# Kernel optimization log

Hardware: AMD Instinct MI355X
Metric: run time of the kernel (lower is better)

Reference implementation:

```python
import jax, jax.numpy as jnp
import numpy as np

B, T, C, H = 8, 1024, 768, 12
D = C // H  # head_dim = 64

def _rope_tables(seq_len, d, base=10000.0):
    inv_freq = 1.0 / (base ** (jnp.arange(0, d, 2, dtype=jnp.float32) / d))  # [d/2]
    freqs = jnp.outer(jnp.arange(seq_len, dtype=jnp.float32), inv_freq)      # [T, d/2]
    return jnp.cos(freqs), jnp.sin(freqs)

def _apply_rotary(x, cos, sin):
    # x: [B,T,H,D]; cos/sin: [1,T,1,D/2]
    d = x.shape[-1] // 2
    x1, x2 = x[..., :d], x[..., d:]
    return jnp.concatenate([x1 * cos + x2 * sin, -x1 * sin + x2 * cos], axis=-1)

def setup_inputs() -> dict:
    key = jax.random.key(0)
    k1, k2, k3 = jax.random.split(key, 3)
    x = jax.random.normal(k1, (B, T, C), dtype=jnp.float32)
    w_qkv = jax.random.normal(k2, (3 * C, C), dtype=jnp.float32) * (C ** -0.5)
    w_proj = jax.random.normal(k3, (C, C), dtype=jnp.float32) * (C ** -0.5)
    return {"x": x, "w_qkv": w_qkv, "w_proj": w_proj}

def reference(x, w_qkv, w_proj):
    Bb, Tt, Cc = x.shape
    qkv = x @ w_qkv.T                                   # [B,T,3C]
    q, k, v = jnp.split(qkv, 3, axis=2)
    q = q.reshape(Bb, Tt, H, D)
    k = k.reshape(Bb, Tt, H, D)
    v = v.reshape(Bb, Tt, H, D)
    cos, sin = _rope_tables(Tt, D)
    cos = cos[None, :, None, :]
    sin = sin[None, :, None, :]
    q = _apply_rotary(q, cos, sin)
    k = _apply_rotary(k, cos, sin)
    scale = 1.0 / jnp.sqrt(jnp.float32(D))
    scores = jnp.einsum('bthd,bshd->bhts', q, k) * scale  # [B,H,T,T]
    causal = jnp.tril(jnp.ones((Tt, Tt), dtype=bool))
    scores = jnp.where(causal[None, None], scores, jnp.finfo(scores.dtype).min)
    p = jax.nn.softmax(scores, axis=-1)
    y = jnp.einsum('bhts,bshd->bthd', p, v).reshape(Bb, Tt, Cc)
    return y @ w_proj.T
```

## Files before the change

### kernel.cpp

```cpp
#include <hip/hip_runtime.h>
#include <hip/hip_bf16.h>

#define Bb 8
#define Tt 1024
#define Cc 768
#define Hh 12
#define Dd 64
#define M_ROWS (Bb * Tt)
#define QKV_N (3 * Cc)

typedef __attribute__((ext_vector_type(8))) short s16x8;
typedef __attribute__((ext_vector_type(4))) short s16x4;
typedef __attribute__((ext_vector_type(4))) float f32x4;

static __device__ __forceinline__ short f2bf(float f) {
    union { float f; unsigned u; } v; v.f = f;
    unsigned r = (v.u + 0x7fffu + ((v.u >> 16) & 1u)) >> 16;
    return (short)r;
}

__global__ __launch_bounds__(256) void cast_bf16(const float* __restrict__ in,
                                                 short* __restrict__ out, int n8) {
    int i = blockIdx.x * blockDim.x + threadIdx.x;
    if (i >= n8) return;
    const float4 a = ((const float4*)in)[i * 2];
    const float4 b = ((const float4*)in)[i * 2 + 1];
    s16x8 f;
    f[0] = f2bf(a.x); f[1] = f2bf(a.y); f[2] = f2bf(a.z); f[3] = f2bf(a.w);
    f[4] = f2bf(b.x); f[5] = f2bf(b.y); f[6] = f2bf(b.z); f[7] = f2bf(b.w);
    ((s16x8*)out)[i] = f;
}

__global__ __launch_bounds__(256) void rope_tables(float2* __restrict__ cs) {
    int idx = blockIdx.x * blockDim.x + threadIdx.x;
    int t = idx >> 5, i = idx & 31;
    float inv_freq = exp2f(-0.41524101186092037f * (float)i);
    float fr = (float)t * inv_freq;
    float2 v; v.x = cosf(fr); v.y = sinf(fr);
    cs[idx] = v;
}

template <int MODE>
__global__ __launch_bounds__(256) void gemm_nt_mfma(const short* __restrict__ A,
                                                    const short* __restrict__ B,
                                                    void* __restrict__ Cout,
                                                    const float2* __restrict__ cs,
                                                    int M, int N, int K) {
    __shared__ short As[128 * 32];
    __shared__ short Bs[128 * 32];

    const int wave = threadIdx.x >> 6;
    const int lane = threadIdx.x & 63;
    const int l16  = lane & 15;
    const int quad = lane >> 4;
    const int wm = (wave >> 1) * 64;
    const int wn = (wave & 1) * 64;
    const int bm = blockIdx.y * 128;
    const int bn = blockIdx.x * 128;

    f32x4 acc[4][4] = {};

    for (int k0 = 0; k0 < K; k0 += 32) {
        __syncthreads();
#pragma unroll
        for (int i = 0; i < 2; i++) {
            const int idx = (wave * 2 + i) * 64 + lane;
            const int row = idx >> 2;
            const int kc  = (idx & 3) * 8;
            const short* ga = A + (size_t)(bm + row) * K + k0 + kc;
            const short* gb = B + (size_t)(bn + row) * K + k0 + kc;
            __builtin_amdgcn_global_load_lds(
                (const __attribute__((address_space(1))) unsigned*)ga,
                (__attribute__((address_space(3))) unsigned*)&As[(wave * 2 + i) * 512],
                16, 0, 0);
            __builtin_amdgcn_global_load_lds(
                (const __attribute__((address_space(1))) unsigned*)gb,
                (__attribute__((address_space(3))) unsigned*)&Bs[(wave * 2 + i) * 512],
                16, 0, 0);
        }
        __syncthreads();

        s16x8 af[4], bfr[4];
#pragma unroll
        for (int mt = 0; mt < 4; mt++)
            af[mt] = *(const s16x8*)&As[(wm + mt * 16 + l16) * 32 + quad * 8];
#pragma unroll
        for (int nt = 0; nt < 4; nt++)
            bfr[nt] = *(const s16x8*)&Bs[(wn + nt * 16 + l16) * 32 + quad * 8];
#pragma unroll
        for (int mt = 0; mt < 4; mt++)
#pragma unroll
            for (int nt = 0; nt < 4; nt++)
                acc[mt][nt] = __builtin_amdgcn_mfma_f32_16x16x32_bf16(
                    af[mt], bfr[nt], acc[mt][nt], 0, 0, 0);
    }

    if constexpr (MODE == 0) {
#pragma unroll
        for (int mt = 0; mt < 4; mt++)
#pragma unroll
            for (int r = 0; r < 4; r++) {
                const size_t row = bm + wm + mt * 16 + quad * 4 + r;
#pragma unroll
                for (int nt = 0; nt < 4; nt++)
                    ((float*)Cout)[row * N + bn + wn + nt * 16 + l16] = acc[mt][nt][r];
            }
    } else {
        const bool is_v = (bn >= 2 * Cc);
        if (is_v) {
#pragma unroll
            for (int mt = 0; mt < 4; mt++)
#pragma unroll
                for (int r = 0; r < 4; r++) {
                    const size_t row = bm + wm + mt * 16 + quad * 4 + r;
#pragma unroll
                    for (int nt = 0; nt < 4; nt++)
                        ((short*)Cout)[row * N + bn + wn + nt * 16 + l16] = f2bf(acc[mt][nt][r]);
                }
        } else {
            const float scale = (bn < Cc) ? 0.125f : 1.0f;
#pragma unroll
            for (int mt = 0; mt < 4; mt++) {
#pragma unroll
                for (int r = 0; r < 4; r++) {
                    const int row = bm + wm + mt * 16 + quad * 4 + r;
                    const int t = row & (Tt - 1);
                    const float2 c0 = cs[t * 32 + l16];
                    const float2 c1 = cs[t * 32 + 16 + l16];
                    const float x0 = acc[mt][0][r], x1 = acc[mt][1][r];
                    const float x2 = acc[mt][2][r], x3 = acc[mt][3][r];
                    short* cp = (short*)Cout + (size_t)row * N + bn + wn;
                    cp[l16]      = f2bf((x0 * c0.x + x2 * c0.y) * scale);
                    cp[16 + l16] = f2bf((x1 * c1.x + x3 * c1.y) * scale);
                    cp[32 + l16] = f2bf((-x0 * c0.y + x2 * c0.x) * scale);
                    cp[48 + l16] = f2bf((-x1 * c1.y + x3 * c1.x) * scale);
                }
            }
        }
    }
}

#define KSP 72
#define VSP 72
#define PP  76

__global__ __launch_bounds__(256) void flash_attn(const short* __restrict__ qkv,
                                                  short* __restrict__ y) {
    __shared__ short Ks[2][64 * KSP];
    __shared__ short Vs[2][Dd * VSP];
    __shared__ short Ps[4][16 * PP];

    const int wave = threadIdx.x >> 6;
    const int lane = threadIdx.x & 63;
    const int l16  = lane & 15;
    const int quad = lane >> 4;

    const int pair = blockIdx.x / 96;
    const int bh   = blockIdx.x % 96;
    const int h = bh % Hh;
    const int b = bh / Hh;
    const int qa_blk = pair;
    const int qb_blk = 15 - pair;
    const int q0a = qa_blk * 64 + wave * 16;
    const int q0b = qb_blk * 64 + wave * 16;

    s16x8 qfa[2], qfb[2];
    {
        const short* qpa = qkv + (size_t)(b * Tt + q0a + l16) * QKV_N + h * Dd + quad * 8;
        const short* qpb = qkv + (size_t)(b * Tt + q0b + l16) * QKV_N + h * Dd + quad * 8;
        qfa[0] = *(const s16x8*)qpa;  qfa[1] = *(const s16x8*)(qpa + 32);
        qfb[0] = *(const s16x8*)qpb;  qfb[1] = *(const s16x8*)(qpb + 32);
    }

    f32x4 oa[4] = {}, ob[4] = {};
    float la[4] = {0.f, 0.f, 0.f, 0.f}, lb[4] = {0.f, 0.f, 0.f, 0.f};

    short* pw = &Ps[wave][0];

    const int krow = threadIdx.x >> 2;
    const int kd0  = (threadIdx.x & 3) * 16;
    const int key2 = (threadIdx.x & 31) * 2;
    const int dv0  = (threadIdx.x >> 5) * 8;

    s16x8 pk0, pk1, pv0, pv1;
    auto load_tile = [&](int kbase) {
        const short* kp = qkv + (size_t)(b * Tt + kbase + krow) * QKV_N + Cc + h * Dd + kd0;
        pk0 = *(const s16x8*)kp;
        pk1 = *(const s16x8*)(kp + 8);
        const short* vp = qkv + (size_t)(b * Tt + kbase + key2) * QKV_N + 2 * Cc + h * Dd + dv0;
        pv0 = *(const s16x8*)vp;
        pv1 = *(const s16x8*)(vp + QKV_N);
    };
    auto store_tile = [&](int buf) {
        *(s16x8*)&Ks[buf][krow * KSP + kd0]     = pk0;
        *(s16x8*)&Ks[buf][krow * KSP + kd0 + 8] = pk1;
#pragma unroll
        for (int j = 0; j < 8; j++) {
            ushort2 w; w.x = (unsigned short)pv0[j]; w.y = (unsigned short)pv1[j];
            *(ushort2*)&Vs[buf][(dv0 + j) * VSP + key2] = w;
        }
    };

    auto process = [&](int buf, int q0, const s16x8* qf, f32x4* o, float* l_r,
                       int kbase, bool masked) {
        f32x4 sv[4];
#pragma unroll
        for (int g = 0; g < 4; g++) {
            s16x8 kf0 = *(const s16x8*)&Ks[buf][(g * 16 + l16) * KSP + quad * 8];
            s16x8 kf1 = *(const s16x8*)&Ks[buf][(g * 16 + l16) * KSP + 32 + quad * 8];
            f32x4 z = {};
            z = __builtin_amdgcn_mfma_f32_16x16x32_bf16(qf[0], kf0, z, 0, 0, 0);
            z = __builtin_amdgcn_mfma_f32_16x16x32_bf16(qf[1], kf1, z, 0, 0, 0);
            sv[g] = z;
        }
#pragma unroll
        for (int r = 0; r < 4; r++) {
            const int qg = q0 + quad * 4 + r;
            float rs = 0.f;
#pragma unroll
            for (int g = 0; g < 4; g++) {
                float p = __expf(sv[g][r]);
                if (masked) p = (kbase + g * 16 + l16 <= qg) ? p : 0.0f;
                rs += p;
                pw[(quad * 4 + r) * PP + g * 16 + l16] = f2bf(p);
            }
            l_r[r] += rs;
        }
#pragma unroll
        for (int c = 0; c < 2; c++) {
            s16x4 plo = *(const s16x4*)&pw[l16 * PP + c * 32 + quad * 8];
            s16x4 phi = *(const s16x4*)&pw[l16 * PP + c * 32 + quad * 8 + 4];
            s16x8 pa = __builtin_shufflevector(plo, phi, 0, 1, 2, 3, 4, 5, 6, 7);
#pragma unroll
            for (int nc = 0; nc < 4; nc++) {
                s16x8 vb = *(const s16x8*)&Vs[buf][(nc * 16 + l16) * VSP + c * 32 + quad * 8];
                o[nc] = __builtin_amdgcn_mfma_f32_16x16x32_bf16(pa, vb, o[nc], 0, 0, 0);
            }
        }
    };

    load_tile(0);
    store_tile(0);
    for (int kt = 0; kt <= qb_blk; kt++) {
        __syncthreads();
        const int nb = (kt < qb_blk) ? (kt + 1) * 64 : qb_blk * 64;
        load_tile(nb);
        const int buf = kt & 1;
        const int kbase = kt * 64;
        process(buf, q0b, qfb, ob, lb, kbase, kt == qb_blk);
        if (kt <= qa_blk)
            process(buf, q0a, qfa, oa, la, kbase, kt == qa_blk);
        store_tile(buf ^ 1);
    }

#pragma unroll
    for (int r = 0; r < 4; r++) {
        float sa = la[r], sb = lb[r];
#pragma unroll
        for (int off = 1; off < 16; off <<= 1) {
            sa += __shfl_xor(sa, off, 64);
            sb += __shfl_xor(sb, off, 64);
        }
        const float inva = 1.0f / sa;
        const float invb = 1.0f / sb;
        short* ypa = y + (size_t)(b * Tt + q0a + quad * 4 + r) * Cc + h * Dd;
        short* ypb = y + (size_t)(b * Tt + q0b + quad * 4 + r) * Cc + h * Dd;
#pragma unroll
        for (int nc = 0; nc < 4; nc++) {
            ypa[nc * 16 + l16] = f2bf(oa[nc][r] * inva);
            ypb[nc * 16 + l16] = f2bf(ob[nc][r] * invb);
        }
    }
}

extern "C" void kernel_launch(void* const* d_in, const int* in_sizes, int n_in,
                              void* d_out, int out_size, void* d_ws, size_t ws_size,
                              hipStream_t stream) {
    const float* x      = (const float*)d_in[0];
    const float* w_qkv  = (const float*)d_in[1];
    const float* w_proj = (const float*)d_in[2];
    float* out = (float*)d_out;

    float2* cs    = (float2*)d_ws;
    short* xb     = (short*)(cs + Tt * 32);
    short* wqkvb  = xb + (size_t)M_ROWS * Cc;
    short* wprojb = wqkvb + (size_t)QKV_N * Cc;
    short* qkvb   = wprojb + (size_t)Cc * Cc;
    short* yb     = qkvb + (size_t)M_ROWS * QKV_N;

    cast_bf16<<<(M_ROWS * Cc / 8 + 255) / 256, 256, 0, stream>>>(x, xb, M_ROWS * Cc / 8);
    cast_bf16<<<(QKV_N * Cc / 8 + 255) / 256, 256, 0, stream>>>(w_qkv, wqkvb, QKV_N * Cc / 8);
    cast_bf16<<<(Cc * Cc / 8 + 255) / 256, 256, 0, stream>>>(w_proj, wprojb, Cc * Cc / 8);
    rope_tables<<<(Tt * 32) / 256, 256, 0, stream>>>(cs);

    gemm_nt_mfma<1><<<dim3(QKV_N / 128, M_ROWS / 128), 256, 0, stream>>>(
        xb, wqkvb, qkvb, cs, M_ROWS, QKV_N, Cc);

    flash_attn<<<96 * 8, 256, 0, stream>>>(qkvb, yb);

    gemm_nt_mfma<0><<<dim3(Cc / 128, M_ROWS / 128), 256, 0, stream>>>(
        yb, wprojb, out, nullptr, M_ROWS, Cc, Cc);
}
```

Before: 199.8 us.

## Fuse prep kernels, deepen GEMM K-tile with swizzled LDS, and remap blocks per XCD

The three bf16 casts and the RoPE table build are merged into one prep kernel, saving launch overhead. Both GEMMs now stage 64-wide K tiles instead of 32, with an XOR swizzle on the LDS column to avoid bank conflicts. They also use a 1D grid remapped so each XCD owns a contiguous band of M row-blocks, for better L2 locality. The larger tiles double LDS use per block, which may lower occupancy, and the attention kernel is unchanged.

```diff
diff --git a/kernel.cpp b/kernel.cpp
--- a/kernel.cpp
+++ b/kernel.cpp
@@ -19,10 +19,8 @@
     return (short)r;
 }
 
-__global__ __launch_bounds__(256) void cast_bf16(const float* __restrict__ in,
-                                                 short* __restrict__ out, int n8) {
-    int i = blockIdx.x * blockDim.x + threadIdx.x;
-    if (i >= n8) return;
+static __device__ __forceinline__ void cast8(const float* __restrict__ in,
+                                             short* __restrict__ out, int i) {
     const float4 a = ((const float4*)in)[i * 2];
     const float4 b = ((const float4*)in)[i * 2 + 1];
     s16x8 f;
@@ -31,13 +29,33 @@
     ((s16x8*)out)[i] = f;
 }
 
-__global__ __launch_bounds__(256) void rope_tables(float2* __restrict__ cs) {
+#define S1 (M_ROWS * Cc / 8)
+#define S2 (QKV_N * Cc / 8)
+#define S3 (Cc * Cc / 8)
+#define SROPE (Tt * 32)
+#define PREP_THREADS (S1 + S2 + S3 + SROPE)
+
+__global__ __launch_bounds__(256) void prep_kernel(const float* __restrict__ x,
+                                                   const float* __restrict__ wqkv,
+                                                   const float* __restrict__ wproj,
+                                                   short* __restrict__ xb,
+                                                   short* __restrict__ wqkvb,
+                                                   short* __restrict__ wprojb,
+                                                   float2* __restrict__ cs) {
     int idx = blockIdx.x * blockDim.x + threadIdx.x;
-    int t = idx >> 5, i = idx & 31;
-    float inv_freq = exp2f(-0.41524101186092037f * (float)i);
-    float fr = (float)t * inv_freq;
-    float2 v; v.x = cosf(fr); v.y = sinf(fr);
-    cs[idx] = v;
+    if (idx < S1) { cast8(x, xb, idx); return; }
+    idx -= S1;
+    if (idx < S2) { cast8(wqkv, wqkvb, idx); return; }
+    idx -= S2;
+    if (idx < S3) { cast8(wproj, wprojb, idx); return; }
+    idx -= S3;
+    {
+        int t = idx >> 5, i = idx & 31;
+        float inv_freq = exp2f(-0.41524101186092037f * (float)i);
+        float fr = (float)t * inv_freq;
+        float2 v; v.x = cosf(fr); v.y = sinf(fr);
+        cs[idx] = v;
+    }
 }
 
 template <int MODE>
@@ -45,9 +63,9 @@
                                                     const short* __restrict__ B,
                                                     void* __restrict__ Cout,
                                                     const float2* __restrict__ cs,
-                                                    int M, int N, int K) {
-    __shared__ short As[128 * 32];
-    __shared__ short Bs[128 * 32];
+                                                    int M, int N, int K, int nblocks) {
+    __shared__ short As[128 * 64];
+    __shared__ short Bs[128 * 64];
 
     const int wave = threadIdx.x >> 6;
     const int lane = threadIdx.x & 63;
@@ -55,44 +73,53 @@
     const int quad = lane >> 4;
     const int wm = (wave >> 1) * 64;
     const int wn = (wave & 1) * 64;
-    const int bm = blockIdx.y * 128;
-    const int bn = blockIdx.x * 128;
+
+    const int mb8  = (M >> 7) >> 3;
+    const int xcd  = blockIdx.x & 7;
+    const int slot = blockIdx.x >> 3;
+    const int bm = (xcd * mb8 + slot / nblocks) * 128;
+    const int bn = (slot % nblocks) * 128;
 
     f32x4 acc[4][4] = {};
 
-    for (int k0 = 0; k0 < K; k0 += 32) {
+    for (int k0 = 0; k0 < K; k0 += 64) {
         __syncthreads();
 #pragma unroll
-        for (int i = 0; i < 2; i++) {
-            const int idx = (wave * 2 + i) * 64 + lane;
-            const int row = idx >> 2;
-            const int kc  = (idx & 3) * 8;
-            const short* ga = A + (size_t)(bm + row) * K + k0 + kc;
-            const short* gb = B + (size_t)(bn + row) * K + k0 + kc;
+        for (int j = 0; j < 4; j++) {
+            const int idx = (j * 4 + wave) * 64 + lane;
+            const int row = idx >> 3;
+            const int kc  = (((idx & 7) ^ ((idx >> 3) & 7)) * 8);
             __builtin_amdgcn_global_load_lds(
-                (const __attribute__((address_space(1))) unsigned*)ga,
-                (__attribute__((address_space(3))) unsigned*)&As[(wave * 2 + i) * 512],
+                (const __attribute__((address_space(1))) unsigned*)
+                    (A + (size_t)(bm + row) * K + k0 + kc),
+                (__attribute__((address_space(3))) unsigned*)&As[(j * 4 + wave) * 512],
                 16, 0, 0);
             __builtin_amdgcn_global_load_lds(
-                (const __attribute__((address_space(1))) unsigned*)gb,
-                (__attribute__((address_space(3))) unsigned*)&Bs[(wave * 2 + i) * 512],
+                (const __attribute__((address_space(1))) unsigned*)
+                    (B + (size_t)(bn + row) * K + k0 + kc),
+                (__attribute__((address_space(3))) unsigned*)&Bs[(j * 4 + wave) * 512],
                 16, 0, 0);
         }
         __syncthreads();
 
-        s16x8 af[4], bfr[4];
-#pragma unroll
-        for (int mt = 0; mt < 4; mt++)
-            af[mt] = *(const s16x8*)&As[(wm + mt * 16 + l16) * 32 + quad * 8];
-#pragma unroll
-        for (int nt = 0; nt < 4; nt++)
-            bfr[nt] = *(const s16x8*)&Bs[(wn + nt * 16 + l16) * 32 + quad * 8];
-#pragma unroll
-        for (int mt = 0; mt < 4; mt++)
+#pragma unroll
+        for (int c = 0; c < 2; c++) {
+            const int swz = (l16 & 7) * 8;
+            const int col = (c * 32 + quad * 8) ^ swz;
+            s16x8 af[4], bfr[4];
+#pragma unroll
+            for (int mt = 0; mt < 4; mt++)
+                af[mt] = *(const s16x8*)&As[(wm + mt * 16 + l16) * 64 + col];
 #pragma unroll
             for (int nt = 0; nt < 4; nt++)
-                acc[mt][nt] = __builtin_amdgcn_mfma_f32_16x16x32_bf16(
-                    af[mt], bfr[nt], acc[mt][nt], 0, 0, 0);
+                bfr[nt] = *(const s16x8*)&Bs[(wn + nt * 16 + l16) * 64 + col];
+#pragma unroll
+            for (int mt = 0; mt < 4; mt++)
+#pragma unroll
+                for (int nt = 0; nt < 4; nt++)
+                    acc[mt][nt] = __builtin_amdgcn_mfma_f32_16x16x32_bf16(
+                        af[mt], bfr[nt], acc[mt][nt], 0, 0, 0);
+        }
     }
 
     if constexpr (MODE == 0) {
@@ -288,16 +315,14 @@
     short* qkvb   = wprojb + (size_t)Cc * Cc;
     short* yb     = qkvb + (size_t)M_ROWS * QKV_N;
 
-    cast_bf16<<<(M_ROWS * Cc / 8 + 255) / 256, 256, 0, stream>>>(x, xb, M_ROWS * Cc / 8);
-    cast_bf16<<<(QKV_N * Cc / 8 + 255) / 256, 256, 0, stream>>>(w_qkv, wqkvb, QKV_N * Cc / 8);
-    cast_bf16<<<(Cc * Cc / 8 + 255) / 256, 256, 0, stream>>>(w_proj, wprojb, Cc * Cc / 8);
-    rope_tables<<<(Tt * 32) / 256, 256, 0, stream>>>(cs);
-
-    gemm_nt_mfma<1><<<dim3(QKV_N / 128, M_ROWS / 128), 256, 0, stream>>>(
-        xb, wqkvb, qkvb, cs, M_ROWS, QKV_N, Cc);
+    prep_kernel<<<PREP_THREADS / 256, 256, 0, stream>>>(
+        x, w_qkv, w_proj, xb, wqkvb, wprojb, cs);
+
+    gemm_nt_mfma<1><<<(QKV_N / 128) * (M_ROWS / 128), 256, 0, stream>>>(
+        xb, wqkvb, qkvb, cs, M_ROWS, QKV_N, Cc, QKV_N / 128);
 
     flash_attn<<<96 * 8, 256, 0, stream>>>(qkvb, yb);
 
-    gemm_nt_mfma<0><<<dim3(Cc / 128, M_ROWS / 128), 256, 0, stream>>>(
-        yb, wprojb, out, nullptr, M_ROWS, Cc, Cc);
-}
+    gemm_nt_mfma<0><<<(Cc / 128) * (M_ROWS / 128), 256, 0, stream>>>(
+        yb, wprojb, out, nullptr, M_ROWS, Cc, Cc, Cc / 128);
+}
```

After: 187.7 us. -6.1%, faster.
